# Kernel tuning notes

Measured on AMD Instinct MI355X. Metric: run time of the kernel, lower is better.

The kernel has to match this reference:

```python
import jax, jax.numpy as jnp
import numpy as np

N = 100000        # num nodes
E = 3200000       # num edges (avg degree 32)
F_IN = 256        # num_features
H = 8             # hidden_channels
C = 16            # num_classes
NEG_SLOPE = 0.2   # GATv2Conv default negative_slope


def setup_inputs() -> dict:
    key = jax.random.key(0)
    ks = jax.random.split(key, 14)
    s = 0.1
    return {
        "x": jax.random.normal(ks[0], (N, F_IN), dtype=jnp.float32),
        "edge_index": jax.random.randint(ks[1], (2, E), 0, N),
        # layer 1 (GATv2Conv: lin_l for source, lin_r for target, att vector, out bias)
        "Wl1": jax.random.normal(ks[2], (F_IN, H), jnp.float32) * s,
        "bl1": jnp.zeros((H,), jnp.float32),
        "Wr1": jax.random.normal(ks[3], (F_IN, H), jnp.float32) * s,
        "br1": jnp.zeros((H,), jnp.float32),
        "att1": jax.random.normal(ks[4], (H,), jnp.float32) * s,
        "bias1": jnp.zeros((H,), jnp.float32),
        # layer 2
        "Wl2": jax.random.normal(ks[5], (H, C), jnp.float32) * s,
        "bl2": jnp.zeros((C,), jnp.float32),
        "Wr2": jax.random.normal(ks[6], (H, C), jnp.float32) * s,
        "br2": jnp.zeros((C,), jnp.float32),
        "att2": jax.random.normal(ks[7], (C,), jnp.float32) * s,
        "bias2": jnp.zeros((C,), jnp.float32),
    }


def _gatv2_conv(x, src, dst, Wl, bl, Wr, br, att, bias, n):
    # PyG GATv2Conv (heads=1): x_l = lin_l(x) (source), x_r = lin_r(x) (target)
    xl = x @ Wl + bl                                   # [N, D]
    xr = x @ Wr + br                                   # [N, D]
    e = jax.nn.leaky_relu(xl[src] + xr[dst], NEG_SLOPE)  # [E+N, D]
    s = e @ att                                        # [E+N] attention logits
    # softmax over incoming edges of each target node (segment softmax)
    m = jax.ops.segment_max(s, dst, num_segments=n)
    ex = jnp.exp(s - m[dst])
    denom = jax.ops.segment_sum(ex, dst, num_segments=n)
    alpha = ex / denom[dst]                            # [E+N]
    out = jax.ops.segment_sum(xl[src] * alpha[:, None], dst, num_segments=n)
    return out + bias


def reference(x, edge_index, Wl1, bl1, Wr1, br1, att1, bias1,
              Wl2, bl2, Wr2, br2, att2, bias2):
    # add_self_loops=True (GATv2Conv default)
    loop = jnp.arange(N, dtype=edge_index.dtype)
    src = jnp.concatenate([edge_index[0], loop])
    dst = jnp.concatenate([edge_index[1], loop])
    h = jax.nn.relu(_gatv2_conv(x, src, dst, Wl1, bl1, Wr1, br1, att1, bias1, N))
    return _gatv2_conv(h, src, dst, Wl2, bl2, Wr2, br2, att2, bias2, N)
```

## Files before the change

### kernel.cpp

```cpp
#include <hip/hip_runtime.h>

#define NN 100000
#define NE 3200000
#define FIN 256
#define H1 8
#define C2 16
#define NEG 0.2f

#define BKT 64
#define NB 1563
#define NBP 1568
#define CAP 2560
#define SB 32
#define SBN 3136
#define FPS 49
#define SCAP 110000
#define P1B 1024
#define EPB1 3125
#define LINB 1563
#define P2CAP 3520

__global__ __launch_bounds__(512) void k_clr(int* __restrict__ g) {
    int i = blockIdx.x * 512 + threadIdx.x;
    if (i < SB + NBP) g[i] = 0;
}

__global__ __launch_bounds__(512) void k_b(
        const float* __restrict__ x,
        const float* __restrict__ Wl, const float* __restrict__ bl,
        const float* __restrict__ Wr, const float* __restrict__ br,
        float* __restrict__ xl1, float* __restrict__ xr1,
        const int* __restrict__ ei,
        int* __restrict__ gcur1, int* __restrict__ sup1) {
    __shared__ int smem[10240];
    int tid = threadIdx.x;
    int m = blockIdx.x % 5, d = blockIdx.x / 5;

    if (m >= 3) {
        int p1 = d * 2 + (m - 3);
        if (p1 >= P1B) return;
        int* buf  = smem;
        int* cnt  = smem + EPB1;
        int* nb   = cnt + SB;
        int* cnt2 = nb + SB;
        int* gb   = cnt2 + SB;
        int base = p1 * EPB1;
        if (tid < SB) { cnt[tid] = 0; cnt2[tid] = 0; }
        int es[7], ed[7];
        #pragma unroll
        for (int r = 0; r < 7; ++r) {
            int i = tid + r * 512;
            if (i < EPB1) { es[r] = ei[base + i]; ed[r] = ei[NE + base + i]; }
        }
        __syncthreads();
        #pragma unroll
        for (int r = 0; r < 7; ++r) {
            int i = tid + r * 512;
            if (i < EPB1) atomicAdd(&cnt[ed[r] / SBN], 1);
        }
        __syncthreads();
        if (tid < SB) {
            int v = cnt[tid], inc = v;
            #pragma unroll
            for (int off = 1; off < SB; off <<= 1) {
                int u = __shfl_up(inc, off, 64);
                if (tid >= off) inc += u;
            }
            nb[tid] = inc - v;
            gb[tid] = atomicAdd(&gcur1[tid], v);
        }
        __syncthreads();
        #pragma unroll
        for (int r = 0; r < 7; ++r) {
            int i = tid + r * 512;
            if (i < EPB1) {
                int s = ed[r] / SBN;
                int rr = ed[r] - s * SBN;
                int k = atomicAdd(&cnt2[s], 1);
                buf[nb[s] + k] = (rr << 17) | es[r];
            }
        }
        __syncthreads();
        for (int j = tid; j < EPB1; j += 512) {
            int s = 0;
            #pragma unroll
            for (int st = 16; st >= 1; st >>= 1) {
                int c = s + st;
                if (c < SB && nb[c] <= j) s = c;
            }
            int dst = gb[s] + (j - nb[s]);
            if (dst < SCAP) sup1[(size_t)s * SCAP + dst] = buf[j];
        }
    } else {
        int lb = d * 3 + m;
        if (lb >= LINB) return;
        int blkNode = lb * 64;
        float* xf   = (float*)smem;
        float* part = (float*)smem;
        int lane = tid & 63;
        int wq = __builtin_amdgcn_readfirstlane(tid >> 6);

        float accl[8] = {0,0,0,0,0,0,0,0}, accr[8] = {0,0,0,0,0,0,0,0};

        #pragma unroll
        for (int ph = 0; ph < 2; ++ph) {
            __syncthreads();
            #pragma unroll
            for (int pass = 0; pass < 4; ++pass) {
                int i = tid + pass * 512;
                int row = i >> 5, c4 = i & 31;
                int node = blkNode + row; if (node >= NN) node = NN - 1;
                float4 v = *(const float4*)(x + (size_t)node * FIN + ph * 128 + c4 * 4);
                *(float4*)&xf[row * 128 + ((c4 ^ (row & 7)) << 2)] = v;
            }
            __syncthreads();
            int kbase = ph * 128 + wq * 16;
            const float* wlp = Wl + kbase * 8;
            const float* wrp = Wr + kbase * 8;
            const float* xbase = &xf[lane * 128];
            int lsw = lane & 7;
            #pragma unroll
            for (int jq = 0; jq < 4; ++jq) {
                int f = wq * 4 + jq;
                float4 xv = *(const float4*)(xbase + ((f ^ lsw) << 2));
                float xa[4] = {xv.x, xv.y, xv.z, xv.w};
                #pragma unroll
                for (int r = 0; r < 4; ++r) {
                    int k = jq * 4 + r;
                    #pragma unroll
                    for (int h = 0; h < 8; ++h) {
                        accl[h] = fmaf(xa[r], wlp[k * 8 + h], accl[h]);
                        accr[h] = fmaf(xa[r], wrp[k * 8 + h], accr[h]);
                    }
                }
            }
        }
        __syncthreads();
        float* pw = part + (size_t)(wq * 64 + lane) * 20;
        *(float4*)(pw)      = make_float4(accl[0], accl[1], accl[2], accl[3]);
        *(float4*)(pw + 4)  = make_float4(accl[4], accl[5], accl[6], accl[7]);
        *(float4*)(pw + 8)  = make_float4(accr[0], accr[1], accr[2], accr[3]);
        *(float4*)(pw + 12) = make_float4(accr[4], accr[5], accr[6], accr[7]);
        __syncthreads();
        int n2 = tid >> 3, p = tid & 7;
        float s0 = 0.f, s1 = 0.f;
        #pragma unroll
        for (int w2 = 0; w2 < 8; ++w2) {
            const float* pr = part + (size_t)(w2 * 64 + n2) * 20 + p * 2;
            s0 += pr[0]; s1 += pr[1];
        }
        int node = blkNode + n2;
        if (node < NN) {
            int o = p * 2;
            if (o < 8) {
                s0 += bl[o]; s1 += bl[o + 1];
                *(float2*)(xl1 + (size_t)node * H1 + o) = make_float2(s0, s1);
            } else {
                s0 += br[o - 8]; s1 += br[o - 7];
                *(float2*)(xr1 + (size_t)node * H1 + (o - 8)) = make_float2(s0, s1);
            }
        }
    }
}

__global__ __launch_bounds__(512) void k_p2(const int* __restrict__ sup1,
                                            const int* __restrict__ gcur1,
                                            int* __restrict__ gcur2,
                                            int* __restrict__ bedges) {
    __shared__ int buf[P2CAP];
    __shared__ int cnt[FPS], nb[FPS], cnt2[FPS], gb[FPS];
    int s   = blockIdx.x >> 5;
    int sub = blockIdx.x & 31;
    int tid = threadIdx.x;
    int total = gcur1[s]; if (total > SCAP) total = SCAP;
    int beg = (int)((long)total * sub / 32);
    int end = (int)((long)total * (sub + 1) / 32);
    int n = end - beg;
    const int* sp = sup1 + (size_t)s * SCAP + beg;
    if (tid < FPS) { cnt[tid] = 0; cnt2[tid] = 0; }
    int pk[7];
    #pragma unroll
    for (int r = 0; r < 7; ++r) {
        int i = tid + r * 512;
        if (i < n) pk[r] = sp[i];
    }
    __syncthreads();
    #pragma unroll
    for (int r = 0; r < 7; ++r) {
        int i = tid + r * 512;
        if (i < n) atomicAdd(&cnt[(pk[r] >> 17) >> 6], 1);
    }
    __syncthreads();
    if (tid < 64) {
        int v = (tid < FPS) ? cnt[tid] : 0, inc = v;
        #pragma unroll
        for (int off = 1; off < 64; off <<= 1) {
            int u = __shfl_up(inc, off, 64);
            if (tid >= off) inc += u;
        }
        if (tid < FPS) {
            nb[tid] = inc - v;
            gb[tid] = atomicAdd(&gcur2[s * FPS + tid], v);
        }
    }
    __syncthreads();
    #pragma unroll
    for (int r = 0; r < 7; ++r) {
        int i = tid + r * 512;
        if (i < n) {
            int fb = (pk[r] >> 17) >> 6;
            int k = atomicAdd(&cnt2[fb], 1);
            buf[nb[fb] + k] = (((pk[r] >> 17) & 63) << 17) | (pk[r] & 0x1FFFF);
        }
    }
    __syncthreads();
    for (int j = tid; j < n; j += 512) {
        int fb = 0;
        #pragma unroll
        for (int st = 32; st >= 1; st >>= 1) {
            int c = fb + st;
            if (c < FPS && nb[c] <= j) fb = c;
        }
        int dst = gb[fb] + (j - nb[fb]);
        if (dst < CAP) bedges[(size_t)(s * FPS + fb) * CAP + dst] = buf[j];
    }
}

__global__ __launch_bounds__(512) void k_sortgat1(
        int* __restrict__ bedges, const int* __restrict__ gcur2,
        int* __restrict__ meta,
        const float* __restrict__ xl, const float* __restrict__ xr,
        const float* __restrict__ att, const float* __restrict__ bias,
        const float* __restrict__ Wl2, const float* __restrict__ bl2,
        const float* __restrict__ Wr2, const float* __restrict__ br2,
        float* __restrict__ xl2, float* __restrict__ xr2) {
    __shared__ int sorted[CAP];
    __shared__ int hist[BKT], nbase[BKT], scnt[BKT];
    int bkt = blockIdx.x;
    int tid = threadIdx.x;
    int ecnt = gcur2[bkt]; if (ecnt > CAP) ecnt = CAP;
    int* be = bedges + (size_t)bkt * CAP;
    if (tid < BKT) { hist[tid] = 0; scnt[tid] = 0; }
    __syncthreads();
    int pkc[5];
    {
        int r = 0;
        for (int i = tid; i < ecnt; i += 512, ++r) {
            pkc[r] = be[i];
            atomicAdd(&hist[pkc[r] >> 17], 1);
        }
    }
    __syncthreads();
    if (tid < BKT) {
        int v = hist[tid], inc = v;
        #pragma unroll
        for (int off = 1; off < 64; off <<= 1) {
            int u = __shfl_up(inc, off, 64);
            if (tid >= off) inc += u;
        }
        nbase[tid] = inc - v;
        meta[bkt * BKT + tid] = ((inc - v) << 16) | v;
    }
    __syncthreads();
    {
        int r = 0;
        for (int i = tid; i < ecnt; i += 512, ++r) {
            int pk = pkc[r];
            int dl = pk >> 17;
            int k = atomicAdd(&scnt[dl], 1);
            sorted[nbase[dl] + k] = pk & 0x1FFFF;
        }
    }
    __syncthreads();
    for (int i = tid; i < ecnt; i += 512)
        be[i] = sorted[i];

    int lane = tid & 63, wave = tid >> 6;
    int grp  = lane >> 4;
    int l16  = lane & 15;
    int q    = l16 & 1;
    int eo   = l16 >> 1;

    float attq[4], biasq[4];
    #pragma unroll
    for (int j = 0; j < 4; ++j) { attq[j] = att[q * 4 + j]; biasq[j] = bias[q * 4 + j]; }
    float wl2c[H1], wr2c[H1];
    #pragma unroll
    for (int d = 0; d < H1; ++d) {
        wl2c[d] = Wl2[d * C2 + l16];
        wr2c[d] = Wr2[d * C2 + l16];
    }
    float bl2c = bl2[l16], br2c = br2[l16];

    #pragma unroll
    for (int np = 0; np < 2; ++np) {
        int n = np * 32 + wave * 4 + grp;
        int g = bkt * BKT + n;
        int gc = g < NN ? g : NN - 1;
        int deg = hist[n] + 1;
        int nb_ = nbase[n];

        float4 xr4 = ((const float4*)(xr + (size_t)gc * H1))[q];
        float xrq[4] = {xr4.x, xr4.y, xr4.z, xr4.w};

        float denom = 0.f;
        float acc[4] = {0.f, 0.f, 0.f, 0.f};
        int mc = (deg + 7) >> 3;

        for (int c = 0; c < mc; ++c) {
            int e = c * 8 + eo;
            int src = (e > 0 && e < deg) ? sorted[nb_ + e - 1] : gc;
            float4 v = ((const float4*)(xl + (size_t)src * H1))[q];
            float xa[4] = {v.x, v.y, v.z, v.w};
            float s = 0.f;
            #pragma unroll
            for (int j = 0; j < 4; ++j) {
                float w = xa[j] + xrq[j];
                w = fmaxf(w, NEG * w);
                s = fmaf(attq[j], w, s);
            }
            s += __shfl_xor(s, 1, 64);
            float ex = (e < deg) ? __expf(s) : 0.f;
            denom += ex;
            #pragma unroll
            for (int j = 0; j < 4; ++j)
                acc[j] = fmaf(ex, xa[j], acc[j]);
        }

        #pragma unroll
        for (int off = 2; off <= 8; off <<= 1) {
            denom += __shfl_xor(denom, off, 64);
            #pragma unroll
            for (int j = 0; j < 4; ++j)
                acc[j] += __shfl_xor(acc[j], off, 64);
        }
        float inv = 1.f / denom;

        float h[4];
        #pragma unroll
        for (int j = 0; j < 4; ++j)
            h[j] = fmaxf(acc[j] * inv + biasq[j], 0.f);
        float hd[H1];
        #pragma unroll
        for (int d = 0; d < H1; ++d)
            hd[d] = __shfl(h[d & 3], (lane & 0x30) + (d >> 2), 64);
        float al = bl2c, ar = br2c;
        #pragma unroll
        for (int d = 0; d < H1; ++d) {
            al = fmaf(hd[d], wl2c[d], al);
            ar = fmaf(hd[d], wr2c[d], ar);
        }
        if (g < NN) {
            xl2[(size_t)g * C2 + l16] = al;
            xr2[(size_t)g * C2 + l16] = ar;
        }
    }
}

__global__ __launch_bounds__(128) void k_gat2L(
        const int* __restrict__ sorted_g, const int* __restrict__ meta,
        const float* __restrict__ xl, const float* __restrict__ xr,
        const float* __restrict__ att, const float* __restrict__ bias,
        float* __restrict__ out) {
    int wv = (blockIdx.x * 128 + threadIdx.x) >> 6;
    int gbase = __builtin_amdgcn_readfirstlane(wv << 2);
    int lane = threadIdx.x & 63;
    int q = lane & 3, eo = lane >> 2;

    float attq[4], biasq[4];
    #pragma unroll
    for (int j = 0; j < 4; ++j) { attq[j] = att[q * 4 + j]; biasq[j] = bias[q * 4 + j]; }

    #pragma unroll 2
    for (int i = 0; i < 4; ++i) {
        int g = gbase + i;
        int mt = meta[g];
        int deg = (mt & 0xFFFF) + 1;
        const int* sg = sorted_g + (size_t)(g >> 6) * CAP + (mt >> 16);

        float4 xr4 = ((const float4*)(xr + (size_t)g * C2))[q];
        float xrq[4] = {xr4.x, xr4.y, xr4.z, xr4.w};

        float denom = 0.f;
        float acc[4] = {0.f, 0.f, 0.f, 0.f};

        #pragma unroll
        for (int c = 0; c < 4; ++c) {
            if (c == 0 || deg > c * 16) {
                int e = c * 16 + eo;
                int src = (e > 0 && e < deg) ? sg[e - 1] : g;
                float4 v = ((const float4*)(xl + (size_t)src * C2))[q];
                float xv[4] = {v.x, v.y, v.z, v.w};
                float s = 0.f;
                #pragma unroll
                for (int j = 0; j < 4; ++j) {
                    float w = xv[j] + xrq[j];
                    w = fmaxf(w, NEG * w);
                    s = fmaf(attq[j], w, s);
                }
                s += __shfl_xor(s, 1, 64);
                s += __shfl_xor(s, 2, 64);
                float ex = (e < deg) ? __expf(s) : 0.f;
                denom += ex;
                #pragma unroll
                for (int j = 0; j < 4; ++j)
                    acc[j] = fmaf(ex, xv[j], acc[j]);
            }
        }
        for (int e0 = 64; e0 < deg; e0 += 16) {
            int e = e0 + eo;
            int src = (e < deg) ? sg[e - 1] : g;
            float4 v = ((const float4*)(xl + (size_t)src * C2))[q];
            float xv[4] = {v.x, v.y, v.z, v.w};
            float s = 0.f;
            #pragma unroll
            for (int j = 0; j < 4; ++j) {
                float w = xv[j] + xrq[j];
                w = fmaxf(w, NEG * w);
                s = fmaf(attq[j], w, s);
            }
            s += __shfl_xor(s, 1, 64);
            s += __shfl_xor(s, 2, 64);
            float ex = (e < deg) ? __expf(s) : 0.f;
            denom += ex;
            #pragma unroll
            for (int j = 0; j < 4; ++j)
                acc[j] = fmaf(ex, xv[j], acc[j]);
        }

        #pragma unroll
        for (int off = 4; off < 64; off <<= 1) {
            denom += __shfl_xor(denom, off, 64);
            #pragma unroll
            for (int j = 0; j < 4; ++j)
                acc[j] += __shfl_xor(acc[j], off, 64);
        }
        float inv = 1.f / denom;

        if (eo == 0) {
            float4 r;
            r.x = acc[0] * inv + biasq[0];
            r.y = acc[1] * inv + biasq[1];
            r.z = acc[2] * inv + biasq[2];
            r.w = acc[3] * inv + biasq[3];
            ((float4*)(out + (size_t)g * C2))[q] = r;
        }
    }
}

extern "C" void kernel_launch(void* const* d_in, const int* in_sizes, int n_in,
                              void* d_out, int out_size, void* d_ws, size_t ws_size,
                              hipStream_t stream) {
    const float* x     = (const float*)d_in[0];
    const int*   ei    = (const int*)d_in[1];
    const float* Wl1   = (const float*)d_in[2];
    const float* bl1   = (const float*)d_in[3];
    const float* Wr1   = (const float*)d_in[4];
    const float* br1   = (const float*)d_in[5];
    const float* att1  = (const float*)d_in[6];
    const float* bias1 = (const float*)d_in[7];
    const float* Wl2   = (const float*)d_in[8];
    const float* bl2   = (const float*)d_in[9];
    const float* Wr2   = (const float*)d_in[10];
    const float* br2   = (const float*)d_in[11];
    const float* att2  = (const float*)d_in[12];
    const float* bias2 = (const float*)d_in[13];
    float* out = (float*)d_out;

    int* bedges = (int*)d_ws;
    int* gcur1  = bedges + (size_t)NBP * CAP;
    int* gcur2  = gcur1 + SB;
    int* meta   = gcur2 + NBP;
    float* xl1  = (float*)(meta + NBP * BKT);
    float* xr1  = xl1 + (size_t)NN * H1;
    int* sup1   = (int*)(xr1 + (size_t)NN * H1);
    float* xl2  = (float*)sup1;
    float* xr2  = xl2 + (size_t)NN * C2;

    k_clr<<<4, 512, 0, stream>>>(gcur1);
    k_b<<<2605, 512, 0, stream>>>(x, Wl1, bl1, Wr1, br1, xl1, xr1,
                                  ei, gcur1, sup1);
    k_p2<<<1024, 512, 0, stream>>>(sup1, gcur1, gcur2, bedges);
    k_sortgat1<<<NB, 512, 0, stream>>>(bedges, gcur2, meta, xl1, xr1, att1, bias1,
                                       Wl2, bl2, Wr2, br2, xl2, xr2);
    k_gat2L<<<12500, 128, 0, stream>>>(bedges, meta, xl2, xr2, att2, bias2, out);
}
```

Measured before the change: 124.6 us.

## Compute layer-1 linear projection with split-bf16 MFMA instead of scalar FMAs

Replaces the scalar-FMA, LDS-staged x@[Wl|Wr] projection with per-wave 16x16x32 bf16 MFMA tiles. The fp32 precision is approximated by splitting inputs and weights into hi/lo bf16 parts and summing three products. A new pre-kernel converts the weights to transposed hi/lo bf16 arrays and also clears the counters. The block mix in k_b is rebalanced to four partition blocks per three linear blocks, and shared memory shrinks. This aims to cut the ALU cost of the projection so the kernel is bound by streaming x, at the risk of small accuracy differences from dropping the lo*lo term.

```diff
diff --git a/kernel.cpp b/kernel.cpp
--- a/kernel.cpp
+++ b/kernel.cpp
@@ -17,27 +17,44 @@
 #define SCAP 110000
 #define P1B 1024
 #define EPB1 3125
-#define LINB 1563
+#define LINB 782
+#define NTILE 6250
 #define P2CAP 3520
 
-__global__ __launch_bounds__(512) void k_clr(int* __restrict__ g) {
+typedef __attribute__((ext_vector_type(8))) short bf16x8;
+typedef __attribute__((ext_vector_type(4))) float f32x4;
+
+__global__ __launch_bounds__(512) void k_pre(
+        int* __restrict__ gcur,
+        const float* __restrict__ Wl, const float* __restrict__ Wr,
+        unsigned short* __restrict__ Bth, unsigned short* __restrict__ Btlo) {
     int i = blockIdx.x * 512 + threadIdx.x;
-    if (i < SB + NBP) g[i] = 0;
+    if (i < SB + NBP) gcur[i] = 0;
+    if (i < 4096) {
+        int n = i >> 8, k = i & 255;
+        float v = (n < 8) ? Wl[k * 8 + n] : Wr[k * 8 + (n - 8)];
+        unsigned u = __float_as_uint(v);
+        unsigned h = u & 0xFFFF0000u;
+        float lo = v - __uint_as_float(h);
+        Bth[i]  = (unsigned short)(u >> 16);
+        Btlo[i] = (unsigned short)(__float_as_uint(lo) >> 16);
+    }
 }
 
 __global__ __launch_bounds__(512) void k_b(
         const float* __restrict__ x,
-        const float* __restrict__ Wl, const float* __restrict__ bl,
-        const float* __restrict__ Wr, const float* __restrict__ br,
+        const unsigned short* __restrict__ Bth,
+        const unsigned short* __restrict__ Btlo,
+        const float* __restrict__ bl, const float* __restrict__ br,
         float* __restrict__ xl1, float* __restrict__ xr1,
         const int* __restrict__ ei,
         int* __restrict__ gcur1, int* __restrict__ sup1) {
-    __shared__ int smem[10240];
+    __shared__ int smem[3328];
     int tid = threadIdx.x;
-    int m = blockIdx.x % 5, d = blockIdx.x / 5;
+    int m = blockIdx.x % 7, d = blockIdx.x / 7;
 
     if (m >= 3) {
-        int p1 = d * 2 + (m - 3);
+        int p1 = d * 4 + (m - 3);
         if (p1 >= P1B) return;
         int* buf  = smem;
         int* cnt  = smem + EPB1;
@@ -94,72 +111,46 @@
     } else {
         int lb = d * 3 + m;
         if (lb >= LINB) return;
-        int blkNode = lb * 64;
-        float* xf   = (float*)smem;
-        float* part = (float*)smem;
-        int lane = tid & 63;
-        int wq = __builtin_amdgcn_readfirstlane(tid >> 6);
-
-        float accl[8] = {0,0,0,0,0,0,0,0}, accr[8] = {0,0,0,0,0,0,0,0};
-
-        #pragma unroll
-        for (int ph = 0; ph < 2; ++ph) {
-            __syncthreads();
-            #pragma unroll
-            for (int pass = 0; pass < 4; ++pass) {
-                int i = tid + pass * 512;
-                int row = i >> 5, c4 = i & 31;
-                int node = blkNode + row; if (node >= NN) node = NN - 1;
-                float4 v = *(const float4*)(x + (size_t)node * FIN + ph * 128 + c4 * 4);
-                *(float4*)&xf[row * 128 + ((c4 ^ (row & 7)) << 2)] = v;
-            }
-            __syncthreads();
-            int kbase = ph * 128 + wq * 16;
-            const float* wlp = Wl + kbase * 8;
-            const float* wrp = Wr + kbase * 8;
-            const float* xbase = &xf[lane * 128];
-            int lsw = lane & 7;
-            #pragma unroll
-            for (int jq = 0; jq < 4; ++jq) {
-                int f = wq * 4 + jq;
-                float4 xv = *(const float4*)(xbase + ((f ^ lsw) << 2));
-                float xa[4] = {xv.x, xv.y, xv.z, xv.w};
-                #pragma unroll
-                for (int r = 0; r < 4; ++r) {
-                    int k = jq * 4 + r;
-                    #pragma unroll
-                    for (int h = 0; h < 8; ++h) {
-                        accl[h] = fmaf(xa[r], wlp[k * 8 + h], accl[h]);
-                        accr[h] = fmaf(xa[r], wrp[k * 8 + h], accr[h]);
-                    }
-                }
-            }
-        }
-        __syncthreads();
-        float* pw = part + (size_t)(wq * 64 + lane) * 20;
-        *(float4*)(pw)      = make_float4(accl[0], accl[1], accl[2], accl[3]);
-        *(float4*)(pw + 4)  = make_float4(accl[4], accl[5], accl[6], accl[7]);
-        *(float4*)(pw + 8)  = make_float4(accr[0], accr[1], accr[2], accr[3]);
-        *(float4*)(pw + 12) = make_float4(accr[4], accr[5], accr[6], accr[7]);
-        __syncthreads();
-        int n2 = tid >> 3, p = tid & 7;
-        float s0 = 0.f, s1 = 0.f;
-        #pragma unroll
-        for (int w2 = 0; w2 < 8; ++w2) {
-            const float* pr = part + (size_t)(w2 * 64 + n2) * 20 + p * 2;
-            s0 += pr[0]; s1 += pr[1];
-        }
-        int node = blkNode + n2;
-        if (node < NN) {
-            int o = p * 2;
-            if (o < 8) {
-                s0 += bl[o]; s1 += bl[o + 1];
-                *(float2*)(xl1 + (size_t)node * H1 + o) = make_float2(s0, s1);
-            } else {
-                s0 += br[o - 8]; s1 += br[o - 7];
-                *(float2*)(xr1 + (size_t)node * H1 + (o - 8)) = make_float2(s0, s1);
-            }
-        }
+        int wave = tid >> 6, lane = tid & 63;
+        int tile = lb * 8 + wave;
+        if (tile >= NTILE) return;
+        int n16 = lane & 15;
+        int kg  = lane >> 4;
+
+        const float* xp = x + (size_t)(tile * 16 + n16) * FIN + (kg << 3);
+        const unsigned short* bhp = Bth  + n16 * 256 + (kg << 3);
+        const unsigned short* blp = Btlo + n16 * 256 + (kg << 3);
+
+        f32x4 acc = {0.f, 0.f, 0.f, 0.f};
+        #pragma unroll
+        for (int ks = 0; ks < 8; ++ks) {
+            float4 a0 = *(const float4*)(xp + ks * 32);
+            float4 a1 = *(const float4*)(xp + ks * 32 + 4);
+            float f[8] = {a0.x, a0.y, a0.z, a0.w, a1.x, a1.y, a1.z, a1.w};
+            union { int w[4]; bf16x8 v; } ah, al;
+            #pragma unroll
+            for (int p = 0; p < 4; ++p) {
+                unsigned u0 = __float_as_uint(f[2 * p]);
+                unsigned u1 = __float_as_uint(f[2 * p + 1]);
+                unsigned h0 = u0 & 0xFFFF0000u, h1 = u1 & 0xFFFF0000u;
+                ah.w[p] = (int)(h1 | (u0 >> 16));
+                float l0 = f[2 * p]     - __uint_as_float(h0);
+                float l1 = f[2 * p + 1] - __uint_as_float(h1);
+                al.w[p] = (int)((__float_as_uint(l1) & 0xFFFF0000u) |
+                                (__float_as_uint(l0) >> 16));
+            }
+            bf16x8 bh = *(const bf16x8*)(bhp + ks * 32);
+            bf16x8 bo = *(const bf16x8*)(blp + ks * 32);
+            acc = __builtin_amdgcn_mfma_f32_16x16x32_bf16(ah.v, bh, acc, 0, 0, 0);
+            acc = __builtin_amdgcn_mfma_f32_16x16x32_bf16(ah.v, bo, acc, 0, 0, 0);
+            acc = __builtin_amdgcn_mfma_f32_16x16x32_bf16(al.v, bh, acc, 0, 0, 0);
+        }
+        float bias = (n16 < 8) ? bl[n16] : br[n16 - 8];
+        float* dstb = (n16 < 8) ? (xl1 + n16) : (xr1 + (n16 - 8));
+        int nodeb = tile * 16 + kg * 4;
+        #pragma unroll
+        for (int r = 0; r < 4; ++r)
+            dstb[(size_t)(nodeb + r) * H1] = acc[r] + bias;
     }
 }
 
@@ -471,14 +462,16 @@
     int* gcur1  = bedges + (size_t)NBP * CAP;
     int* gcur2  = gcur1 + SB;
     int* meta   = gcur2 + NBP;
-    float* xl1  = (float*)(meta + NBP * BKT);
+    unsigned short* Bth  = (unsigned short*)(meta + NBP * BKT);
+    unsigned short* Btlo = Bth + 4096;
+    float* xl1  = (float*)(Btlo + 4096);
     float* xr1  = xl1 + (size_t)NN * H1;
     int* sup1   = (int*)(xr1 + (size_t)NN * H1);
     float* xl2  = (float*)sup1;
     float* xr2  = xl2 + (size_t)NN * C2;
 
-    k_clr<<<4, 512, 0, stream>>>(gcur1);
-    k_b<<<2605, 512, 0, stream>>>(x, Wl1, bl1, Wr1, br1, xl1, xr1,
+    k_pre<<<8, 512, 0, stream>>>(gcur1, Wl1, Wr1, Bth, Btlo);
+    k_b<<<1827, 512, 0, stream>>>(x, Bth, Btlo, bl1, br1, xl1, xr1,
                                   ei, gcur1, sup1);
     k_p2<<<1024, 512, 0, stream>>>(sup1, gcur1, gcur2, bedges);
     k_sortgat1<<<NB, 512, 0, stream>>>(bedges, gcur2, meta, xl1, xr1, att1, bias1,
```

New measurement: 138.4 us. +11.1%, slower.
